# Performance work log

Measured on AMD Instinct MI355X. Metric: run time of the kernel, lower is better.

## Reference

```python
import jax, jax.numpy as jnp
import jax.lax as lax
import numpy as np

# ---- Parallel3DGeometry constants ----
B, C = 1, 1
D, H, W = 64, 96, 96          # internal volume layout (z, y, x)
V, U, A = 64, 96, 90          # detector rows, detector cols, projection angles
SX = SY = SD = 1.0            # voxel size (x, y, z)
SU = SV = 1.0                 # detector spacing
NSTEPS = H + W + 2            # upper bound on voxels crossed by an XY ray
DIAG = float(np.sqrt(SX * SX + SY * SY))
EPS = 1e-12


def _t_for(p0, dp, pmin, pmax):
    # slab entry/exit parameters, matching torch _t_for (incl. parallel-ray cases)
    par = jnp.abs(dp) < EPS
    safe = jnp.where(par, 1.0, dp)
    t0 = (pmin - p0) / safe
    t1 = (pmax - p0) / safe
    lo = jnp.minimum(t0, t1)
    hi = jnp.maximum(t0, t1)
    inside = (p0 >= pmin) & (p0 <= pmax)
    lo = jnp.where(par, jnp.where(inside, -jnp.inf, jnp.inf), lo)
    hi = jnp.where(par, jnp.where(inside, jnp.inf, -jnp.inf), hi)
    return lo, hi


def _trace():
    """Vectorized Siddon XY traversal for all A*U rays.

    Returns Is, Js (int32 [A,U,NSTEPS]) voxel indices and Ws (f32 [A,U,NSTEPS])
    segment lengths (0 where the ray has exited / padded steps).
    """
    angles = jnp.linspace(0.0, np.pi, A, endpoint=False).astype(jnp.float32)
    cos_t = jnp.cos(angles)
    sin_t = jnp.sin(angles)
    u = (jnp.arange(U, dtype=jnp.float32) - (U - 1) / 2.0) * SU
    dx = jnp.broadcast_to(cos_t[:, None], (A, U)).reshape(-1)
    dy = jnp.broadcast_to(sin_t[:, None], (A, U)).reshape(-1)
    x0 = (-u[None, :] * sin_t[:, None]).reshape(-1)
    y0 = (u[None, :] * cos_t[:, None]).reshape(-1)

    x_min = -((W - 1) / 2.0) * SX; x_max = ((W - 1) / 2.0) * SX
    y_min = -((H - 1) / 2.0) * SY; y_max = ((H - 1) / 2.0) * SY
    tx0, tx1 = _t_for(x0, dx, x_min, x_max)
    ty0, ty1 = _t_for(y0, dy, y_min, y_max)
    t_entry = jnp.maximum(tx0, ty0)
    t_exit = jnp.minimum(tx1, ty1)
    alive0 = t_entry < t_exit
    te = jnp.where(alive0, t_entry, 0.0)
    tex = jnp.where(alive0, t_exit, 0.0)
    xe = x0 + te * dx
    ye = y0 + te * dy
    i0 = jnp.clip(jnp.round(xe / SX + (W - 1) / 2.0), 0, W - 1).astype(jnp.int32)
    j0 = jnp.clip(jnp.round(ye / SY + (H - 1) / 2.0), 0, H - 1).astype(jnp.int32)
    cxw = (W - 1) / 2.0 * SX
    cyh = (H - 1) / 2.0 * SY

    def body(st, _):
        i, j, x, y, t, alive = st
        valid = alive & (t < tex - EPS)
        fi = i.astype(jnp.float32)
        fj = j.astype(jnp.float32)
        xn = jnp.where(dx > 0, (fi + 0.5) * SX - cxw,
                       jnp.where(dx < 0, (fi - 0.5) * SX - cxw, jnp.inf))
        yn = jnp.where(dy > 0, (fj + 0.5) * SY - cyh,
                       jnp.where(dy < 0, (fj - 0.5) * SY - cyh, jnp.inf))
        okx = jnp.abs(dx) > EPS
        oky = jnp.abs(dy) > EPS
        tx = jnp.where(okx, (xn - x) / jnp.where(okx, dx, 1.0), jnp.inf)
        ty = jnp.where(oky, (yn - y) / jnp.where(oky, dy, 1.0), jnp.inf)
        dt = jnp.minimum(jnp.minimum(tx, ty), tex - t)
        seg = jnp.maximum(0.0, dt * DIAG / jnp.maximum(jnp.abs(dx) + jnp.abs(dy), EPS))
        w = jnp.where(valid, seg, 0.0)
        i_n = i + jnp.where(tx <= ty, jnp.where(dx > 0, 1, -1), 0)
        j_n = j + jnp.where(ty <= tx, jnp.where(dy > 0, 1, -1), 0)
        inb = (i_n >= 0) & (i_n < W) & (j_n >= 0) & (j_n < H)
        dts = jnp.where(valid, dt, 0.0)
        st2 = (jnp.where(valid, i_n, i), jnp.where(valid, j_n, j),
               x + dx * dts, y + dy * dts, t + dts, valid & inb)
        return st2, (i, j, w)

    init = (i0, j0, xe, ye, te, alive0)
    _, (Is, Js, Ws) = lax.scan(body, init, None, length=NSTEPS)
    # [NSTEPS, R] -> [A, U, NSTEPS]
    Is = Is.T.reshape(A, U, NSTEPS)
    Js = Js.T.reshape(A, U, NSTEPS)
    Ws = Ws.T.reshape(A, U, NSTEPS)
    return Is, Js, Ws


def _forward(vol):
    # model-facing [B,C,X,Y,Z] -> internal [B,C,D,H,W]
    vol_int = jnp.transpose(vol, (0, 1, 4, 3, 2))
    Is, Js, Ws = _trace()
    v_phys = (jnp.arange(V, dtype=jnp.float32) - (V - 1) / 2.0) * SV
    k = jnp.clip(jnp.round(v_phys / SD + (D - 1) / 2.0), 0, D - 1).astype(jnp.int32)
    # gather voxel values along every ray: [B,C,V,A,U,NSTEPS]
    g = vol_int[:, :, k[:, None, None, None], Js[None], Is[None]]
    out = jnp.einsum('bcvaun,aun->bcvau', g, Ws.astype(vol.dtype))
    # internal [B,C,V,A,U] (== out[b,c,a,v,u] reordered) -> model-facing [B,C,U,A,V]
    return jnp.transpose(out, (0, 1, 4, 3, 2))


def setup_inputs() -> dict:
    key = jax.random.key(0)
    vol = jax.random.normal(key, (B, C, W, H, D), dtype=jnp.float32)
    return {"vol": vol}


def reference(vol):
    return _forward(vol)
```

## Files before the change

### kernel.cpp

```cpp
#include <hip/hip_runtime.h>
#include <math.h>

namespace {
constexpr int NA = 90, NU = 96, NV = 64, NW = 96, NH = 96, ND = 64;
constexpr int NRAY   = NA * NU;
constexpr int NENT   = 256;
constexpr int CNTMAX = 208;
constexpr int TILE   = 8;
constexpr int NBLK   = 1024;
constexpr int NEXTRA = NRAY - NBLK * TILE;
}

__device__ inline void sincos_poly(double xd, float* s, float* c)
{
    const double INV_PIO2 = 0.63661977236758134308;
    const double PIO2_HI  = 1.57079632679489655800e+00;
    const double PIO2_LO  = 6.12323399573676603587e-17;
    const double qd = rint(xd * INV_PIO2);
    const double r  = (xd - qd * PIO2_HI) - qd * PIO2_LO;
    const double z  = r * r;
    const double sp = r + (r * z) * (-1.66666666666666324348e-01 + z *
                     ( 8.33333333332248946124e-03 + z *
                     (-1.98412698298579493134e-04 + z *
                     ( 2.75573137070700676789e-06 + z *
                     (-2.50507602534068634195e-08 + z *
                       1.58969099521155010221e-10)))));
    const double cp = 1.0 + z * (-0.5 + z *
                     ( 4.16666666666666019037e-02 + z *
                     (-1.38888888888741095749e-03 + z *
                     ( 2.48015872894767294178e-05 + z *
                     (-2.75573143513906633035e-07 + z *
                     ( 2.08757232129817482790e-09 + z *
                      -1.13596475577881948265e-11))))));
    const int q = (int)qd;
    const double sv = (q == 0) ? sp : ((q == 1) ? cp : -sp);
    const double cv = (q == 0) ? cp : ((q == 1) ? -sp : -cp);
    *s = (float)sv;
    *c = (float)cv;
}

__device__ __forceinline__ float rflf(float x) {
    return __int_as_float(__builtin_amdgcn_readfirstlane(__float_as_int(x)));
}
__device__ __forceinline__ int rfli(int x) {
    return __builtin_amdgcn_readfirstlane(x);
}

__device__ __forceinline__ void do_ray(const float* __restrict__ vol,
                                       float* __restrict__ out,
                                       int2* __restrict__ myRow,
                                       const int ray, const int lane)
{
    const int a = ray / NU;
    const int u = ray - a * NU;

    const float EPSf = 1e-12f;
    const float INFp = __builtin_inff();
    const float DIAG = 1.41421356237309514547f;

    const float ang = (float)a * (float)(3.14159265358979323846 / 90.0);
    float dy, dx;
    sincos_poly((double)ang, &dy, &dx);
    const float uu = (float)u - 47.5f;
    const float x0 = __fmul_rn(-uu, dy);
    const float y0 = __fmul_rn( uu, dx);

    const float xmin = -47.5f, xmax = 47.5f;
    const float ymin = -47.5f, ymax = 47.5f;

    float tx0, tx1;
    {
        const bool par = fabsf(dx) < EPSf;
        const float safe = par ? 1.0f : dx;
        const float t0 = __fdiv_rn(xmin - x0, safe);
        const float t1 = __fdiv_rn(xmax - x0, safe);
        const float lo = fminf(t0, t1), hi = fmaxf(t0, t1);
        const bool inside = (x0 >= xmin) && (x0 <= xmax);
        tx0 = par ? (inside ? -INFp : INFp) : lo;
        tx1 = par ? (inside ?  INFp : -INFp) : hi;
    }
    float ty0, ty1;
    {
        const bool par = fabsf(dy) < EPSf;
        const float safe = par ? 1.0f : dy;
        const float t0 = __fdiv_rn(ymin - y0, safe);
        const float t1 = __fdiv_rn(ymax - y0, safe);
        const float lo = fminf(t0, t1), hi = fmaxf(t0, t1);
        const bool inside = (y0 >= ymin) && (y0 <= ymax);
        ty0 = par ? (inside ? -INFp : INFp) : lo;
        ty1 = par ? (inside ?  INFp : -INFp) : hi;
    }

    const float t_entry = fmaxf(tx0, ty0);
    const float t_exit  = fminf(tx1, ty1);
    const bool  alive0  = t_entry < t_exit;
    const float te  = rflf(alive0 ? t_entry : 0.0f);
    const float tex = rflf(alive0 ? t_exit  : 0.0f);

    const float xe = __fadd_rn(x0, __fmul_rn(te, dx));
    const float ye = __fadd_rn(y0, __fmul_rn(te, dy));
    const int i0 = rfli((int)fminf(fmaxf(rintf(__fadd_rn(xe, 47.5f)), 0.0f), 95.0f));
    const int j0 = rfli((int)fminf(fmaxf(rintf(__fadd_rn(ye, 47.5f)), 0.0f), 95.0f));

    const bool okx = fabsf(dx) > EPSf;
    const bool oky = fabsf(dy) > EPSf;
    const float inv_dx = okx ? __fdiv_rn(1.0f, dx) : 0.0f;
    const float inv_dy = oky ? __fdiv_rn(1.0f, dy) : 0.0f;
    const float wscale = rflf(__fdiv_rn(DIAG, fmaxf(fabsf(dx) + fabsf(dy), EPSf)));
    const float tex_m_eps = rflf(__fadd_rn(tex, -EPSf));

    const float cx = (dx > 0.0f) ? -47.0f : -48.0f;
    const float cy = (dy > 0.0f) ? -47.0f : -48.0f;
    const float Ax = rflf(okx ? __fadd_rn(te, __fmul_rn(((float)i0 + cx) - xe, inv_dx)) : INFp);
    const float Ay = rflf(oky ? __fadd_rn(te, __fmul_rn(((float)j0 + cy) - ye, inv_dy)) : INFp);
    const float px = rflf(okx ? fabsf(inv_dx) : 0.0f);
    const float py = rflf(oky ? fabsf(inv_dy) : 0.0f);
    const int   si = rfli((dx > 0.0f) ? 1 : -1);
    const int   sj = rfli((dy > 0.0f) ? 1 : -1);

    const float inv_pq = rflf(__fdiv_rn(1.0f, px + py));
    const float Cc = rflf(Ay - Ax);

    int nx = 0, ny = 0;
    if (okx) {
        const float Qx = __fdiv_rn(tex_m_eps - Ax, px);
        nx = min(96, max(0, (int)floorf(Qx) + 1));
    }
    if (oky) {
        const float Qy = __fdiv_rn(tex_m_eps - Ay, py);
        ny = min(96, max(0, (int)floorf(Qy) + 1));
    }
    const int nvalid = 1 + nx + ny;
    const int rounds = rfli(alive0 ? min(4, (nvalid + 2 + 63) >> 6) : 0);

    int cnt = 0;
    for (int rnd = 0; rnd < rounds; ++rnd) {
        const int n = (rnd << 6) + lane;
        const float nf = (float)n;

        float kf = __fmul_rn(__fmaf_rn(nf, py, Cc), inv_pq);
        kf = fminf(fmaxf(kf, 0.0f), nf);
        int k = (int)rintf(kf);

        #pragma unroll
        for (int it = 0; it < 4; ++it) {
            const int m = n - k;
            const float Txk   = __fmaf_rn((float)k, px, Ax);
            const float Txkm1 = (k > 0) ? __fmaf_rn((float)(k - 1), px, Ax) : -INFp;
            const float Tyl   = __fmaf_rn((float)m, py, Ay);
            const float Tylm1 = (m > 0) ? __fmaf_rn((float)(m - 1), py, Ay) : -INFp;
            const bool dec = (Txkm1 > Tyl);
            const bool inc = (!dec) && (Tylm1 > Txk);
            k += inc ? 1 : (dec ? -1 : 0);
        }

        const int m = n - k;
        const float Txk   = __fmaf_rn((float)k, px, Ax);
        const float Txkm1 = (k > 0) ? __fmaf_rn((float)(k - 1), px, Ax) : -INFp;
        const float Tyl   = __fmaf_rn((float)m, py, Ay);
        const float Tylm1 = (m > 0) ? __fmaf_rn((float)(m - 1), py, Ay) : -INFp;

        const float Tn   = fminf(Txk, Tyl);
        const float prev = fmaxf(te, fmaxf(Txkm1, Tylm1));
        const float dt   = __fadd_rn(fminf(Tn, tex), -fminf(prev, tex));
        const bool active = (prev < tex_m_eps);
        float w = __fmul_rn(fmaxf(0.0f, dt), wscale);
        w = active ? w : 0.0f;

        const int ii = min(95, max(0, i0 + ((si > 0) ? k : -k)));
        const int jj = min(95, max(0, j0 + ((sj > 0) ? m : -m)));
        int2 e;
        e.x = (ii * NH + jj) << 8;
        e.y = __float_as_int(w);
        myRow[n] = e;

        cnt += (int)__popcll(__ballot(active));
    }
    const int cap = min((cnt + 15) & ~15, CNTMAX);

    const int r   = lane >> 4;
    const int sub = lane & 15;
    const int subOff = sub << 4;

    const int2* __restrict__ eRow = myRow + r;
    const char* __restrict__ vb   = (const char*)vol;

    float4 acc[4] = {{0,0,0,0}, {0,0,0,0}, {0,0,0,0}, {0,0,0,0}};
    for (int n = 0; n < cap; n += 16) {
        const int2 e0 = eRow[n];
        const int2 e1 = eRow[n + 4];
        const int2 e2 = eRow[n + 8];
        const int2 e3 = eRow[n + 12];
        const float4 v0 = *(const float4*)(vb + (e0.x + subOff));
        const float4 v1 = *(const float4*)(vb + (e1.x + subOff));
        const float4 v2 = *(const float4*)(vb + (e2.x + subOff));
        const float4 v3 = *(const float4*)(vb + (e3.x + subOff));
        const float w0 = __int_as_float(e0.y);
        const float w1 = __int_as_float(e1.y);
        const float w2 = __int_as_float(e2.y);
        const float w3 = __int_as_float(e3.y);
        acc[0].x = fmaf(w0, v0.x, acc[0].x); acc[0].y = fmaf(w0, v0.y, acc[0].y);
        acc[0].z = fmaf(w0, v0.z, acc[0].z); acc[0].w = fmaf(w0, v0.w, acc[0].w);
        acc[1].x = fmaf(w1, v1.x, acc[1].x); acc[1].y = fmaf(w1, v1.y, acc[1].y);
        acc[1].z = fmaf(w1, v1.z, acc[1].z); acc[1].w = fmaf(w1, v1.w, acc[1].w);
        acc[2].x = fmaf(w2, v2.x, acc[2].x); acc[2].y = fmaf(w2, v2.y, acc[2].y);
        acc[2].z = fmaf(w2, v2.z, acc[2].z); acc[2].w = fmaf(w2, v2.w, acc[2].w);
        acc[3].x = fmaf(w3, v3.x, acc[3].x); acc[3].y = fmaf(w3, v3.y, acc[3].y);
        acc[3].z = fmaf(w3, v3.z, acc[3].z); acc[3].w = fmaf(w3, v3.w, acc[3].w);
    }

    float sx = (acc[0].x + acc[1].x) + (acc[2].x + acc[3].x);
    float sy = (acc[0].y + acc[1].y) + (acc[2].y + acc[3].y);
    float sz = (acc[0].z + acc[1].z) + (acc[2].z + acc[3].z);
    float sw = (acc[0].w + acc[1].w) + (acc[2].w + acc[3].w);

    sx += __shfl_xor(sx, 16, 64);  sy += __shfl_xor(sy, 16, 64);
    sz += __shfl_xor(sz, 16, 64);  sw += __shfl_xor(sw, 16, 64);
    sx += __shfl_xor(sx, 32, 64);  sy += __shfl_xor(sy, 32, 64);
    sz += __shfl_xor(sz, 32, 64);  sw += __shfl_xor(sw, 32, 64);

    if (lane < 16) {
        float4 res; res.x = sx; res.y = sy; res.z = sz; res.w = sw;
        *(float4*)(out + (u * NA + a) * NV + (sub << 2)) = res;
    }
}

__global__ __launch_bounds__(512, 8)
void siddon_fused(const float* __restrict__ vol, float* __restrict__ out)
{
    __shared__ int2 sEnt[TILE][NENT];

    const int tid  = threadIdx.x;
    const int wid  = tid >> 6;
    const int lane = tid & 63;
    const int bid  = blockIdx.x;

    int2* __restrict__ myRow = &sEnt[wid][0];

    const int ray0 = bid * TILE + wid;
    do_ray(vol, out, myRow, ray0, lane);

    if (bid < NEXTRA && wid == ((bid + (bid >> 8)) & 7)) {
        do_ray(vol, out, myRow, NBLK * TILE + bid, lane);
    }
}

extern "C" void kernel_launch(void* const* d_in, const int* in_sizes, int n_in,
                              void* d_out, int out_size, void* d_ws, size_t ws_size,
                              hipStream_t stream) {
    const float* vol = (const float*)d_in[0];
    float* out = (float*)d_out;
    hipLaunchKernelGGL(siddon_fused, dim3(NBLK), dim3(512), 0, stream, vol, out);
}
```

Baseline: 67.14 us.

## Stage volume as fp16 in workspace and gather half-precision columns

Adds a pre-pass kernel that converts the float32 volume to fp16 in the workspace buffer, then has the Siddon gather read 16-byte chunks of 8 half values per lane. Each lane group now covers 8 lanes per ray step instead of 16, with 32 steps per iteration and 8 accumulators per lane. The aim is to halve gather bandwidth and cache footprint for the voxel reads. In exchange it adds a second launch and rounds inputs to fp16, which may break tolerance. It also raises CNTMAX, changing the cap on ray steps processed.

```diff
diff --git a/kernel.cpp b/kernel.cpp
--- a/kernel.cpp
+++ b/kernel.cpp
@@ -1,11 +1,13 @@
 #include <hip/hip_runtime.h>
+#include <hip/hip_fp16.h>
 #include <math.h>
 
 namespace {
 constexpr int NA = 90, NU = 96, NV = 64, NW = 96, NH = 96, ND = 64;
 constexpr int NRAY   = NA * NU;
+constexpr int NVOX   = NW * NH * ND;
 constexpr int NENT   = 256;
-constexpr int CNTMAX = 208;
+constexpr int CNTMAX = 224;
 constexpr int TILE   = 8;
 constexpr int NBLK   = 1024;
 constexpr int NEXTRA = NRAY - NBLK * TILE;
@@ -46,7 +48,25 @@
     return __builtin_amdgcn_readfirstlane(x);
 }
 
-__device__ __forceinline__ void do_ray(const float* __restrict__ vol,
+__global__ __launch_bounds__(256)
+void vol_half_stage(const float* __restrict__ vol, __half* __restrict__ hvol)
+{
+    const int i8 = (blockIdx.x * 256 + threadIdx.x) << 3;
+    const float4 f0 = *(const float4*)(vol + i8);
+    const float4 f1 = *(const float4*)(vol + i8 + 4);
+    __half2 a0 = __floats2half2_rn(f0.x, f0.y);
+    __half2 a1 = __floats2half2_rn(f0.z, f0.w);
+    __half2 a2 = __floats2half2_rn(f1.x, f1.y);
+    __half2 a3 = __floats2half2_rn(f1.z, f1.w);
+    uint4 q;
+    q.x = *(const unsigned int*)&a0;
+    q.y = *(const unsigned int*)&a1;
+    q.z = *(const unsigned int*)&a2;
+    q.w = *(const unsigned int*)&a3;
+    *(uint4*)((char*)hvol + ((size_t)i8 << 1)) = q;
+}
+
+__device__ __forceinline__ void do_ray(const __half* __restrict__ hvol,
                                        float* __restrict__ out,
                                        int2* __restrict__ myRow,
                                        const int ray, const int lane)
@@ -170,63 +190,68 @@
         const int ii = min(95, max(0, i0 + ((si > 0) ? k : -k)));
         const int jj = min(95, max(0, j0 + ((sj > 0) ? m : -m)));
         int2 e;
-        e.x = (ii * NH + jj) << 8;
+        e.x = (ii * NH + jj) << 7;
         e.y = __float_as_int(w);
         myRow[n] = e;
 
         cnt += (int)__popcll(__ballot(active));
     }
-    const int cap = min((cnt + 15) & ~15, CNTMAX);
-
-    const int r   = lane >> 4;
-    const int sub = lane & 15;
+    const int cap = min((cnt + 31) & ~31, CNTMAX);
+
+    const int r   = lane >> 3;
+    const int sub = lane & 7;
     const int subOff = sub << 4;
 
     const int2* __restrict__ eRow = myRow + r;
-    const char* __restrict__ vb   = (const char*)vol;
-
-    float4 acc[4] = {{0,0,0,0}, {0,0,0,0}, {0,0,0,0}, {0,0,0,0}};
-    for (int n = 0; n < cap; n += 16) {
+    const char* __restrict__ hb   = (const char*)hvol;
+
+    float accA[8] = {0,0,0,0,0,0,0,0};
+    float accB[8] = {0,0,0,0,0,0,0,0};
+    for (int n = 0; n < cap; n += 32) {
         const int2 e0 = eRow[n];
-        const int2 e1 = eRow[n + 4];
-        const int2 e2 = eRow[n + 8];
-        const int2 e3 = eRow[n + 12];
-        const float4 v0 = *(const float4*)(vb + (e0.x + subOff));
-        const float4 v1 = *(const float4*)(vb + (e1.x + subOff));
-        const float4 v2 = *(const float4*)(vb + (e2.x + subOff));
-        const float4 v3 = *(const float4*)(vb + (e3.x + subOff));
+        const int2 e1 = eRow[n + 8];
+        const int2 e2 = eRow[n + 16];
+        const int2 e3 = eRow[n + 24];
+        union { uint4 q; __half h[8]; } U0, U1, U2, U3;
+        U0.q = *(const uint4*)(hb + (e0.x + subOff));
+        U1.q = *(const uint4*)(hb + (e1.x + subOff));
+        U2.q = *(const uint4*)(hb + (e2.x + subOff));
+        U3.q = *(const uint4*)(hb + (e3.x + subOff));
         const float w0 = __int_as_float(e0.y);
         const float w1 = __int_as_float(e1.y);
         const float w2 = __int_as_float(e2.y);
         const float w3 = __int_as_float(e3.y);
-        acc[0].x = fmaf(w0, v0.x, acc[0].x); acc[0].y = fmaf(w0, v0.y, acc[0].y);
-        acc[0].z = fmaf(w0, v0.z, acc[0].z); acc[0].w = fmaf(w0, v0.w, acc[0].w);
-        acc[1].x = fmaf(w1, v1.x, acc[1].x); acc[1].y = fmaf(w1, v1.y, acc[1].y);
-        acc[1].z = fmaf(w1, v1.z, acc[1].z); acc[1].w = fmaf(w1, v1.w, acc[1].w);
-        acc[2].x = fmaf(w2, v2.x, acc[2].x); acc[2].y = fmaf(w2, v2.y, acc[2].y);
-        acc[2].z = fmaf(w2, v2.z, acc[2].z); acc[2].w = fmaf(w2, v2.w, acc[2].w);
-        acc[3].x = fmaf(w3, v3.x, acc[3].x); acc[3].y = fmaf(w3, v3.y, acc[3].y);
-        acc[3].z = fmaf(w3, v3.z, acc[3].z); acc[3].w = fmaf(w3, v3.w, acc[3].w);
-    }
-
-    float sx = (acc[0].x + acc[1].x) + (acc[2].x + acc[3].x);
-    float sy = (acc[0].y + acc[1].y) + (acc[2].y + acc[3].y);
-    float sz = (acc[0].z + acc[1].z) + (acc[2].z + acc[3].z);
-    float sw = (acc[0].w + acc[1].w) + (acc[2].w + acc[3].w);
-
-    sx += __shfl_xor(sx, 16, 64);  sy += __shfl_xor(sy, 16, 64);
-    sz += __shfl_xor(sz, 16, 64);  sw += __shfl_xor(sw, 16, 64);
-    sx += __shfl_xor(sx, 32, 64);  sy += __shfl_xor(sy, 32, 64);
-    sz += __shfl_xor(sz, 32, 64);  sw += __shfl_xor(sw, 32, 64);
-
-    if (lane < 16) {
-        float4 res; res.x = sx; res.y = sy; res.z = sz; res.w = sw;
-        *(float4*)(out + (u * NA + a) * NV + (sub << 2)) = res;
+        #pragma unroll
+        for (int z = 0; z < 8; ++z) {
+            accA[z] = fmaf(w0, __half2float(U0.h[z]), accA[z]);
+            accB[z] = fmaf(w1, __half2float(U1.h[z]), accB[z]);
+            accA[z] = fmaf(w2, __half2float(U2.h[z]), accA[z]);
+            accB[z] = fmaf(w3, __half2float(U3.h[z]), accB[z]);
+        }
+    }
+
+    float s[8];
+    #pragma unroll
+    for (int z = 0; z < 8; ++z) s[z] = accA[z] + accB[z];
+
+    #pragma unroll
+    for (int z = 0; z < 8; ++z) {
+        s[z] += __shfl_xor(s[z], 8, 64);
+        s[z] += __shfl_xor(s[z], 16, 64);
+        s[z] += __shfl_xor(s[z], 32, 64);
+    }
+
+    if (lane < 8) {
+        float* op = out + (u * NA + a) * NV + (sub << 3);
+        float4 r0; r0.x = s[0]; r0.y = s[1]; r0.z = s[2]; r0.w = s[3];
+        float4 r1; r1.x = s[4]; r1.y = s[5]; r1.z = s[6]; r1.w = s[7];
+        *(float4*)op = r0;
+        *(float4*)(op + 4) = r1;
     }
 }
 
 __global__ __launch_bounds__(512, 8)
-void siddon_fused(const float* __restrict__ vol, float* __restrict__ out)
+void siddon_fused(const __half* __restrict__ hvol, float* __restrict__ out)
 {
     __shared__ int2 sEnt[TILE][NENT];
 
@@ -238,10 +263,10 @@
     int2* __restrict__ myRow = &sEnt[wid][0];
 
     const int ray0 = bid * TILE + wid;
-    do_ray(vol, out, myRow, ray0, lane);
+    do_ray(hvol, out, myRow, ray0, lane);
 
     if (bid < NEXTRA && wid == ((bid + (bid >> 8)) & 7)) {
-        do_ray(vol, out, myRow, NBLK * TILE + bid, lane);
+        do_ray(hvol, out, myRow, NBLK * TILE + bid, lane);
     }
 }
 
@@ -250,5 +275,8 @@
                               hipStream_t stream) {
     const float* vol = (const float*)d_in[0];
     float* out = (float*)d_out;
-    hipLaunchKernelGGL(siddon_fused, dim3(NBLK), dim3(512), 0, stream, vol, out);
-}
+    __half* hvol = (__half*)d_ws;
+    hipLaunchKernelGGL(vol_half_stage, dim3(NVOX / (256 * 8)), dim3(256), 0, stream,
+                       vol, hvol);
+    hipLaunchKernelGGL(siddon_fused, dim3(NBLK), dim3(512), 0, stream, hvol, out);
+}
```

Measured after the change: 69.99 us. 1.04x slower.
